# Kernel optimization log

Measured on AMD Instinct MI355X. Metric: run time of the kernel, lower is better.

The kernel has to match this reference:

```python
import jax, jax.numpy as jnp
import numpy as np

N, K, D = 100000, 32, 64

def setup_inputs() -> dict:
    key = jax.random.key(0)
    k1, k2, k3 = jax.random.split(key, 3)
    x = jax.random.normal(k1, (N, D), dtype=jnp.float32)
    neighbors = jax.random.randint(k2, (N, K), 0, N, dtype=jnp.int32)
    weights = jax.random.uniform(k3, (N, K), dtype=jnp.float32)
    return {"x": x, "neighbors": neighbors, "weights": weights}

def reference(x, neighbors, weights):
    # Per-node importance pooling: normalize weights over neighbors, then
    # weighted-sum gathered neighbor features. (Vectorized form of the
    # original per-node Python loop; nodes with zero total weight keep
    # unnormalized weights, matching the `if weight_sum > 0` branch.)
    wsum = weights.sum(axis=1, keepdims=True)                 # [N, 1]
    w = jnp.where(wsum > 0, weights / wsum, weights)          # [N, K]
    nbr_feats = x[neighbors]                                  # [N, K, D] gather
    pooled = jnp.einsum("nk,nkd->nd", w, nbr_feats)          # [N, D]
    return pooled
```

## Files before the change

### kernel.cpp

```cpp
#include <hip/hip_runtime.h>
#include <hip/hip_fp16.h>


#define K_NBR 32
#define D_FEAT 64

typedef float vfloat4 __attribute__((ext_vector_type(4)));
typedef unsigned int vuint2 __attribute__((ext_vector_type(2)));

__global__ __launch_bounds__(256) void ImportancePooling_28424093564958_convert(
    const vfloat4* __restrict__ x4, vuint2* __restrict__ xh4, int n4) {
  const int i = blockIdx.x * blockDim.x + threadIdx.x;
  if (i < n4) {
    const vfloat4 v = __builtin_nontemporal_load(x4 + i);
    const __half2 a = __floats2half2_rn(v.x, v.y);
    const __half2 b = __floats2half2_rn(v.z, v.w);
    vuint2 u;
    u.x = *(const unsigned int*)&a;
    u.y = *(const unsigned int*)&b;
    xh4[i] = u;
  }
}

__global__ __launch_bounds__(256) void ImportancePooling_28424093564958_kernel(
    const __half* __restrict__ xh,
    const int* __restrict__ neighbors,
    const float* __restrict__ weights,
    float* __restrict__ out,
    int N) {
  const int wave_id = (int)((blockIdx.x * blockDim.x + threadIdx.x) >> 6);
  const int lane = threadIdx.x & 63;
  if (wave_id >= N) return;

  const long hbase = (long)wave_id * K_NBR;
  int packed;
  if (lane < K_NBR) {
    packed = __float_as_int(__builtin_nontemporal_load(weights + hbase + lane));
  } else {
    packed = __builtin_nontemporal_load(neighbors + hbase + (lane - K_NBR));
  }

  float acc = 0.0f;
  float wsum = 0.0f;
  #pragma unroll
  for (int k = 0; k < K_NBR; ++k) {
    const float wk = __int_as_float(__builtin_amdgcn_readlane(packed, k));
    const int idx = __builtin_amdgcn_readlane(packed, K_NBR + k);
    wsum += wk;
    acc = fmaf(wk, __half2float(xh[(long)idx * D_FEAT + lane]), acc);
  }

  const float inv = (wsum > 0.0f) ? (1.0f / wsum) : 1.0f;
  __builtin_nontemporal_store(acc * inv, out + (long)wave_id * D_FEAT + lane);
}

__global__ __launch_bounds__(256) void ImportancePooling_28424093564958_f32(
    const float* __restrict__ x, const int* __restrict__ neighbors,
    const float* __restrict__ weights, float* __restrict__ out, int N) {
  const int wave_id = (int)((blockIdx.x * blockDim.x + threadIdx.x) >> 6);
  const int lane = threadIdx.x & 63;
  if (wave_id >= N) return;
  const long hbase = (long)wave_id * K_NBR;
  int packed;
  if (lane < K_NBR) {
    packed = __float_as_int(weights[hbase + lane]);
  } else {
    packed = neighbors[hbase + (lane - K_NBR)];
  }
  float acc = 0.0f, wsum = 0.0f;
  #pragma unroll
  for (int k = 0; k < K_NBR; ++k) {
    const float wk = __int_as_float(__builtin_amdgcn_readlane(packed, k));
    const int idx = __builtin_amdgcn_readlane(packed, K_NBR + k);
    wsum += wk;
    acc += wk * x[(long)idx * D_FEAT + lane];
  }
  const float inv = (wsum > 0.0f) ? (1.0f / wsum) : 1.0f;
  out[(long)wave_id * D_FEAT + lane] = acc * inv;
}

extern "C" void kernel_launch(void* const* d_in, const int* in_sizes, int n_in,
                              void* d_out, int out_size, void* d_ws, size_t ws_size,
                              hipStream_t stream) {
  const float* x = (const float*)d_in[0];
  const int* neighbors = (const int*)d_in[1];
  const float* weights = (const float*)d_in[2];
  float* out = (float*)d_out;

  const int N = in_sizes[0] / D_FEAT;
  const int block = 256;
  const int grid = (N * 64 + block - 1) / block;

  const size_t xh_bytes = (size_t)N * D_FEAT * sizeof(__half);
  if (ws_size >= xh_bytes) {
    __half* xh = (__half*)d_ws;
    const int n4 = N * D_FEAT / 4;
    ImportancePooling_28424093564958_convert<<<(n4 + 255) / 256, 256, 0, stream>>>(
        (const vfloat4*)x, (vuint2*)d_ws, n4);
    ImportancePooling_28424093564958_kernel<<<grid, block, 0, stream>>>(
        xh, neighbors, weights, out, N);
  } else {
    ImportancePooling_28424093564958_f32<<<grid, block, 0, stream>>>(
        x, neighbors, weights, out, N);
  }
}
```

Before: 135.7 us.

## Partition feature columns into XCC-affine slices with persistent atomic work queue

Replaces the one-wave-per-node gather with a persistent kernel of 2048 blocks. Each block pulls 128-node chunks from per-slice atomic counters, starting with the column slice that matches its XCC ID, so each XCC's L2 mostly caches one quarter of the fp16 feature table. Each wave now handles 8 nodes at once with 8 lanes per node, loading half2 pairs and broadcasting weights and indices via ds_bpermute. This aims to raise L2 hit rates for the random gathers. The cost is atomic and __syncthreads overhead per chunk, a reliance on the undocumented-in-code XCC mapping, and counters reset inside the convert kernel.

Result: slower. 340.8 us (+151.1%).

```diff
diff --git a/kernel.cpp b/kernel.cpp
--- a/kernel.cpp
+++ b/kernel.cpp
@@ -4,12 +4,17 @@
 
 #define K_NBR 32
 #define D_FEAT 64
+#define CHUNK 128
+#define WS_COUNTER_PAD 256
 
 typedef float vfloat4 __attribute__((ext_vector_type(4)));
+typedef float vfloat2 __attribute__((ext_vector_type(2)));
 typedef unsigned int vuint2 __attribute__((ext_vector_type(2)));
 
 __global__ __launch_bounds__(256) void ImportancePooling_28424093564958_convert(
-    const vfloat4* __restrict__ x4, vuint2* __restrict__ xh4, int n4) {
+    const vfloat4* __restrict__ x4, vuint2* __restrict__ xh4,
+    unsigned int* __restrict__ counters, int n4) {
+  if (blockIdx.x == 0 && threadIdx.x < 8) counters[threadIdx.x] = 0u;
   const int i = blockIdx.x * blockDim.x + threadIdx.x;
   if (i < n4) {
     const vfloat4 v = __builtin_nontemporal_load(x4 + i);
@@ -27,31 +32,73 @@
     const int* __restrict__ neighbors,
     const float* __restrict__ weights,
     float* __restrict__ out,
+    unsigned int* __restrict__ counters,
     int N) {
-  const int wave_id = (int)((blockIdx.x * blockDim.x + threadIdx.x) >> 6);
+  int xcc;
+  asm volatile("s_getreg_b32 %0, hwreg(HW_REG_XCC_ID)" : "=s"(xcc));
   const int lane = threadIdx.x & 63;
-  if (wave_id >= N) return;
+  const int wv = threadIdx.x >> 6;
+  const int j = lane >> 3;
+  const int c = lane & 7;
+  const int vb = (lane & 0x38) << 2;
 
-  const long hbase = (long)wave_id * K_NBR;
-  int packed;
-  if (lane < K_NBR) {
-    packed = __float_as_int(__builtin_nontemporal_load(weights + hbase + lane));
-  } else {
-    packed = __builtin_nontemporal_load(neighbors + hbase + (lane - K_NBR));
+  __shared__ unsigned int sbase;
+
+  for (int s2 = 0; s2 < 4; ++s2) {
+    const int slice = (xcc + s2) & 3;
+    const char* xh_s = (const char*)xh + (slice << 5);
+
+    for (;;) {
+      if (threadIdx.x == 0) sbase = atomicAdd(&counters[slice], (unsigned)CHUNK);
+      __syncthreads();
+      const unsigned base = sbase;
+      __syncthreads();
+      if (base >= (unsigned)N) break;
+
+      #pragma unroll
+      for (int u = 0; u < 4; ++u) {
+        const int n0 = (int)base + wv * 32 + u * 8;
+        const int nj = n0 + j;
+        const bool valid = nj < N;
+        const long hb = (long)(valid ? nj : (N - 1)) * K_NBR;
+
+        float wreg[4];
+        int ireg[4];
+        #pragma unroll
+        for (int m = 0; m < 4; ++m) {
+          wreg[m] = __builtin_nontemporal_load(weights + hb + m * 8 + c);
+          ireg[m] = __builtin_nontemporal_load(neighbors + hb + m * 8 + c);
+        }
+
+        float ws = (wreg[0] + wreg[1]) + (wreg[2] + wreg[3]);
+        ws += __shfl_xor(ws, 1, 64);
+        ws += __shfl_xor(ws, 2, 64);
+        ws += __shfl_xor(ws, 4, 64);
+        const float inv = (ws > 0.0f) ? (1.0f / ws) : 1.0f;
+
+        float ax = 0.0f, ay = 0.0f;
+        #pragma unroll
+        for (int k = 0; k < K_NBR; ++k) {
+          const int m = k >> 3;
+          const int off = (k & 7) << 2;
+          const int wb = __builtin_amdgcn_ds_bpermute(vb + off, __float_as_int(wreg[m]));
+          const int ix = __builtin_amdgcn_ds_bpermute(vb + off, ireg[m]);
+          const float wk = __int_as_float(wb);
+          const __half2 h = *(const __half2*)(xh_s + ((long)(unsigned)ix << 7) + (c << 2));
+          ax = fmaf(wk, __low2float(h), ax);
+          ay = fmaf(wk, __high2float(h), ay);
+        }
+
+        if (valid) {
+          vfloat2 o2;
+          o2.x = ax * inv;
+          o2.y = ay * inv;
+          __builtin_nontemporal_store(
+              o2, (vfloat2*)(out + (long)nj * D_FEAT + (slice << 4) + (c << 1)));
+        }
+      }
+    }
   }
-
-  float acc = 0.0f;
-  float wsum = 0.0f;
-  #pragma unroll
-  for (int k = 0; k < K_NBR; ++k) {
-    const float wk = __int_as_float(__builtin_amdgcn_readlane(packed, k));
-    const int idx = __builtin_amdgcn_readlane(packed, K_NBR + k);
-    wsum += wk;
-    acc = fmaf(wk, __half2float(xh[(long)idx * D_FEAT + lane]), acc);
-  }
-
-  const float inv = (wsum > 0.0f) ? (1.0f / wsum) : 1.0f;
-  __builtin_nontemporal_store(acc * inv, out + (long)wave_id * D_FEAT + lane);
 }
 
 __global__ __launch_bounds__(256) void ImportancePooling_28424093564958_f32(
@@ -88,18 +135,21 @@
   float* out = (float*)d_out;
 
   const int N = in_sizes[0] / D_FEAT;
-  const int block = 256;
-  const int grid = (N * 64 + block - 1) / block;
+  const size_t xh_bytes = (size_t)N * D_FEAT * sizeof(__half);
 
-  const size_t xh_bytes = (size_t)N * D_FEAT * sizeof(__half);
-  if (ws_size >= xh_bytes) {
-    __half* xh = (__half*)d_ws;
+  if (ws_size >= xh_bytes + WS_COUNTER_PAD) {
+    unsigned int* counters = (unsigned int*)d_ws;
+    __half* xh = (__half*)((char*)d_ws + WS_COUNTER_PAD);
+
     const int n4 = N * D_FEAT / 4;
     ImportancePooling_28424093564958_convert<<<(n4 + 255) / 256, 256, 0, stream>>>(
-        (const vfloat4*)x, (vuint2*)d_ws, n4);
-    ImportancePooling_28424093564958_kernel<<<grid, block, 0, stream>>>(
-        xh, neighbors, weights, out, N);
+        (const vfloat4*)x, (vuint2*)xh, counters, n4);
+
+    ImportancePooling_28424093564958_kernel<<<2048, 256, 0, stream>>>(
+        xh, neighbors, weights, out, counters, N);
   } else {
+    const int block = 256;
+    const int grid = (N * 64 + block - 1) / block;
     ImportancePooling_28424093564958_f32<<<grid, block, 0, stream>>>(
         x, neighbors, weights, out, N);
   }
```
